# Performance work log

Measured on AMD Instinct MI355X. Metric: run time of the kernel, lower is better.

The kernel has to match this reference:

```python
import jax, jax.numpy as jnp
import numpy as np
from jax import lax

LATENT, HIDDEN, OUT = 64, 128, 64
B, T = 4096, 100


def setup_inputs() -> dict:
    key = jax.random.key(0)
    ks = jax.random.split(key, 12)
    s = lambda fan_in: 1.0 / np.sqrt(fan_in)
    u = lambda k, shape, fan_in: jax.random.uniform(k, shape, jnp.float32, -s(fan_in), s(fan_in))
    return {
        "z0": jax.random.normal(ks[0], (B, LATENT), jnp.float32),
        "t": jnp.arange(T, dtype=jnp.float32) * 0.01,  # increasing time grid
        "fc1_w": u(ks[1], (HIDDEN, LATENT), LATENT), "fc1_b": u(ks[2], (HIDDEN,), LATENT),
        "fc2_w": u(ks[3], (HIDDEN, HIDDEN), HIDDEN), "fc2_b": u(ks[4], (HIDDEN,), HIDDEN),
        "fc3_w": u(ks[5], (LATENT, HIDDEN), HIDDEN), "fc3_b": u(ks[6], (LATENT,), HIDDEN),
        "l2h_w": u(ks[7], (HIDDEN, LATENT), LATENT), "l2h_b": u(ks[8], (HIDDEN,), LATENT),
        "h2o_w": u(ks[9], (OUT, HIDDEN), HIDDEN), "h2o_b": u(ks[10], (OUT,), HIDDEN),
    }


def reference(z0, t, fc1_w, fc1_b, fc2_w, fc2_b, fc3_w, fc3_b, l2h_w, l2h_b, h2o_w, h2o_b):
    elu = jax.nn.elu

    def f(z):  # ODE_Func: fc1-elu-fc2-elu-fc3
        h = elu(z @ fc1_w.T + fc1_b)
        h = elu(h @ fc2_w.T + fc2_b)
        return h @ fc3_w.T + fc3_b

    dts = t[1:] - t[:-1]  # [T-1]

    def step(z, dt):  # fixed-step RK4
        k1 = f(z)
        k2 = f(z + 0.5 * dt * k1)
        k3 = f(z + 0.5 * dt * k2)
        k4 = f(z + dt * k3)
        zn = z + (dt / 6.0) * (k1 + 2.0 * k2 + 2.0 * k3 + k4)
        return zn, zn

    _, zs = lax.scan(step, z0, dts)          # [T-1, B, latent]
    pred_z = jnp.concatenate([z0[None], zs], axis=0)  # whole sequence [T, B, latent]
    # decode: h2o(relu(l2h(pred_z)))
    h = jax.nn.relu(pred_z @ l2h_w.T + l2h_b)
    return h @ h2o_w.T + h2o_b               # [T, B, out]
```

## Files before the change

### kernel.cpp

```cpp
#include <hip/hip_runtime.h>

typedef _Float16 f16;
typedef _Float16 f16x4 __attribute__((ext_vector_type(4)));
typedef _Float16 f16x8 __attribute__((ext_vector_type(8)));
typedef __fp16   h16x2 __attribute__((ext_vector_type(2)));
typedef float    f32x4 __attribute__((ext_vector_type(4)));

struct h16x2x2 { h16x2 lo, hi; };

#define MFMA16(a,b,c) __builtin_amdgcn_mfma_f32_16x16x32_f16((a),(b),(c),0,0,0)

#define LATENT 64
#define HIDDEN 128
#define ROWB  272
#define ROWF  (ROWB / 2)

__device__ __forceinline__ void bar_lds() {
  asm volatile("s_waitcnt lgkmcnt(0)\n\ts_barrier" ::: "memory");
}

__device__ __forceinline__ f16x8 load_afrag(const float* __restrict__ W, int K,
                                            int tile, int kf, int lane) {
  const int row = tile * 16 + (lane & 15);
  const int k0  = kf * 32 + (lane >> 4) * 8;
  const float* p = W + row * K + k0;
  f16x8 r;
#pragma unroll
  for (int j = 0; j < 8; ++j) r[j] = (f16)p[j];
  return r;
}

__device__ __forceinline__ f16x8 bfrag(const f16* buf, int k0, int lane) {
  const int b  = lane & 15;
  const int kk = k0 + (lane >> 4) * 8;
  return *(const f16x8*)((const char*)buf + b * ROWB + kk * 2);
}

__device__ __forceinline__ void dwrite(f16* buf, int dbase, f32x4 v, int lane) {
  const int b = lane & 15;
  h16x2x2 p;
  p.lo = __builtin_amdgcn_cvt_pkrtz(v[0], v[1]);
  p.hi = __builtin_amdgcn_cvt_pkrtz(v[2], v[3]);
  const f16x4 h = __builtin_bit_cast(f16x4, p);
  *(f16x4*)((char*)buf + b * ROWB + dbase * 2) = h;
}

__device__ __forceinline__ f32x4 elu4(f32x4 d) {
#pragma unroll
  for (int i = 0; i < 4; ++i) {
    const float e = __expf(d[i]) - 1.f;
    d[i] = d[i] > 0.f ? d[i] : e;
  }
  return d;
}

__global__ __launch_bounds__(256, 2)
void node_rk4_kernel(const float* __restrict__ z0,   const float* __restrict__ tg,
                     const float* __restrict__ fc1w, const float* __restrict__ fc1b,
                     const float* __restrict__ fc2w, const float* __restrict__ fc2b,
                     const float* __restrict__ fc3w, const float* __restrict__ fc3b,
                     const float* __restrict__ l2hw, const float* __restrict__ l2hb,
                     const float* __restrict__ h2ow, const float* __restrict__ h2ob,
                     float* __restrict__ out, int Btot, int T) {
  __shared__ __align__(16) f16 xbuf[16 * ROWF];
  __shared__ __align__(16) f16 h1buf[16 * ROWF];
  __shared__ __align__(16) f16 h2buf[16 * ROWF];
  __shared__ __align__(16) f16 dch1[16 * ROWF];

  const int tid  = threadIdx.x;
  const int lane = tid & 63;
  const int wv   = tid >> 6;
  const int grp  = lane >> 4;
  const int bcol = lane & 15;
  const int row0 = blockIdx.x * 16;
  const f32x4 Z0 = {0.f, 0.f, 0.f, 0.f};

  f16x8 a1[2][2], aL[2][2], a2[2][4], a3[4], aO[4];
  f32x4 b1[2], b2[2], bL[2], b3, bO;
#pragma unroll
  for (int ot = 0; ot < 2; ++ot) {
#pragma unroll
    for (int kf = 0; kf < 2; ++kf) {
      a1[ot][kf] = load_afrag(fc1w, 64, 2 * wv + ot, kf, lane);
      aL[ot][kf] = load_afrag(l2hw, 64, 2 * wv + ot, kf, lane);
    }
#pragma unroll
    for (int kf = 0; kf < 4; ++kf) a2[ot][kf] = load_afrag(fc2w, 128, 2 * wv + ot, kf, lane);
    const int d = (2 * wv + ot) * 16 + grp * 4;
    b1[ot] = *(const f32x4*)(fc1b + d);
    b2[ot] = *(const f32x4*)(fc2b + d);
    bL[ot] = *(const f32x4*)(l2hb + d);
  }
#pragma unroll
  for (int kf = 0; kf < 4; ++kf) {
    a3[kf] = load_afrag(fc3w, 128, wv, kf, lane);
    aO[kf] = load_afrag(h2ow, 128, wv, kf, lane);
  }
  const int dz = wv * 16 + grp * 4;
  b3 = *(const f32x4*)(fc3b + dz);
  bO = *(const f32x4*)(h2ob + dz);

  f32x4 z = *(const f32x4*)(z0 + (size_t)(row0 + bcol) * LATENT + dz);

  auto l1 = [&](f16x8 v0, f16x8 v1) {
#pragma unroll
    for (int ot = 0; ot < 2; ++ot) {
      f32x4 d = MFMA16(a1[ot][0], v0, b1[ot]);
      d = MFMA16(a1[ot][1], v1, d);
      d = elu4(d);
      dwrite(h1buf, (2 * wv + ot) * 16 + grp * 4, d, lane);
    }
  };
  auto l2 = [&]() {
    f16x8 h[4];
#pragma unroll
    for (int kf = 0; kf < 4; ++kf) h[kf] = bfrag(h1buf, kf * 32, lane);
#pragma unroll
    for (int ot = 0; ot < 2; ++ot) {
      f32x4 c0 = MFMA16(a2[ot][0], h[0], b2[ot]);
      c0 = MFMA16(a2[ot][1], h[1], c0);
      f32x4 c1 = MFMA16(a2[ot][2], h[2], Z0);
      c1 = MFMA16(a2[ot][3], h[3], c1);
      f32x4 d = elu4(c0 + c1);
      dwrite(h2buf, (2 * wv + ot) * 16 + grp * 4, d, lane);
    }
  };
  auto l3 = [&]() -> f32x4 {
    f16x8 g[4];
#pragma unroll
    for (int kf = 0; kf < 4; ++kf) g[kf] = bfrag(h2buf, kf * 32, lane);
    f32x4 c0 = MFMA16(a3[0], g[0], b3);
    c0 = MFMA16(a3[1], g[1], c0);
    f32x4 c1 = MFMA16(a3[2], g[2], Z0);
    c1 = MFMA16(a3[3], g[3], c1);
    return c0 + c1;
  };
  auto dec2_store = [&](int s) {
    f16x8 hd[4];
#pragma unroll
    for (int kf = 0; kf < 4; ++kf) hd[kf] = bfrag(dch1, kf * 32, lane);
    f32x4 c0 = MFMA16(aO[0], hd[0], bO);
    c0 = MFMA16(aO[1], hd[1], c0);
    f32x4 c1 = MFMA16(aO[2], hd[2], Z0);
    c1 = MFMA16(aO[3], hd[3], c1);
    f32x4 o = c0 + c1;
    *(f32x4*)(out + ((size_t)s * Btot + row0 + bcol) * LATENT + dz) = o;
  };

  dwrite(xbuf, dz, z, lane);
  bar_lds();

  float t_cur = tg[0];
  float t_nxt = tg[1];
  for (int s = 0;; ++s) {
    const bool last = (s == T - 1);

    {
      const f16x8 x0 = bfrag(xbuf, 0, lane);
      const f16x8 x1 = bfrag(xbuf, 32, lane);
#pragma unroll
      for (int ot = 0; ot < 2; ++ot) {
        f32x4 d = MFMA16(aL[ot][0], x0, bL[ot]);
        d = MFMA16(aL[ot][1], x1, d);
#pragma unroll
        for (int i = 0; i < 4; ++i) d[i] = fmaxf(d[i], 0.f);
        dwrite(dch1, (2 * wv + ot) * 16 + grp * 4, d, lane);
      }
      if (!last) l1(x0, x1);
    }
    bar_lds();

    if (last) { dec2_store(s); break; }

    l2();
    bar_lds();

    const float t_fut = tg[s + 2 < T ? s + 2 : T - 1];
    const float dt = t_nxt - t_cur;
    f32x4 k, acc, xs;

    dec2_store(s);
    k = l3();
    acc = k;
#pragma unroll
    for (int i = 0; i < 4; ++i) xs[i] = z[i] + 0.5f * dt * k[i];
    dwrite(xbuf, dz, xs, lane);
    bar_lds();

    { const f16x8 x0 = bfrag(xbuf, 0, lane), x1 = bfrag(xbuf, 32, lane);
      l1(x0, x1); }
    bar_lds();
    l2();
    bar_lds();
    k = l3();
#pragma unroll
    for (int i = 0; i < 4; ++i) { acc[i] += 2.f * k[i]; xs[i] = z[i] + 0.5f * dt * k[i]; }
    dwrite(xbuf, dz, xs, lane);
    bar_lds();

    { const f16x8 x0 = bfrag(xbuf, 0, lane), x1 = bfrag(xbuf, 32, lane);
      l1(x0, x1); }
    bar_lds();
    l2();
    bar_lds();
    k = l3();
#pragma unroll
    for (int i = 0; i < 4; ++i) { acc[i] += 2.f * k[i]; xs[i] = z[i] + dt * k[i]; }
    dwrite(xbuf, dz, xs, lane);
    bar_lds();

    { const f16x8 x0 = bfrag(xbuf, 0, lane), x1 = bfrag(xbuf, 32, lane);
      l1(x0, x1); }
    bar_lds();
    l2();
    bar_lds();
    k = l3();
#pragma unroll
    for (int i = 0; i < 4; ++i) z[i] += (dt / 6.f) * (acc[i] + k[i]);
    dwrite(xbuf, dz, z, lane);
    bar_lds();

    t_cur = t_nxt;
    t_nxt = t_fut;
  }
}

extern "C" void kernel_launch(void* const* d_in, const int* in_sizes, int n_in,
                              void* d_out, int out_size, void* d_ws, size_t ws_size,
                              hipStream_t stream) {
  const float* z0   = (const float*)d_in[0];
  const float* tg   = (const float*)d_in[1];
  const float* fc1w = (const float*)d_in[2];
  const float* fc1b = (const float*)d_in[3];
  const float* fc2w = (const float*)d_in[4];
  const float* fc2b = (const float*)d_in[5];
  const float* fc3w = (const float*)d_in[6];
  const float* fc3b = (const float*)d_in[7];
  const float* l2hw = (const float*)d_in[8];
  const float* l2hb = (const float*)d_in[9];
  const float* h2ow = (const float*)d_in[10];
  const float* h2ob = (const float*)d_in[11];
  float* out = (float*)d_out;

  const int Btot = in_sizes[0] / LATENT;
  const int T    = in_sizes[1];

  dim3 grid(Btot / 16), block(256);
  node_rk4_kernel<<<grid, block, 0, stream>>>(z0, tg, fc1w, fc1b, fc2w, fc2b,
                                              fc3w, fc3b, l2hw, l2hb, h2ow, h2ob,
                                              out, Btot, T);
}
```

Measured before the change: 298.2 us.

## Fold fc3 into fc1 and decoder l2h to track pre-activations instead of z

Precomputes the fused matrices fc1·fc3 and l2h·fc3, plus the bias vectors fc1·b3 and l2h·b3, in the prologue. The RK4 stages then update the fc1 and l2h pre-activations directly from the hidden layer-2 activations, so the separate fc3 and per-stage fc1 GEMMs disappear. The RK4 weighted sum is accumulated in f16 hidden space and applied once per step. This removes one GEMM and barrier pair per stage, but accumulates drift in pre-activation space with f16 rounding of the fused weights and stage sums. Launch bounds drop to one block per SIMD slot, to make room for the larger register footprint.

```diff
diff --git a/kernel.cpp b/kernel.cpp
--- a/kernel.cpp
+++ b/kernel.cpp
@@ -17,6 +17,9 @@
 
 __device__ __forceinline__ void bar_lds() {
   asm volatile("s_waitcnt lgkmcnt(0)\n\ts_barrier" ::: "memory");
+}
+__device__ __forceinline__ void fence_lds() {
+  asm volatile("s_waitcnt lgkmcnt(0)" ::: "memory");
 }
 
 __device__ __forceinline__ f16x8 load_afrag(const float* __restrict__ W, int K,
@@ -54,7 +57,7 @@
   return d;
 }
 
-__global__ __launch_bounds__(256, 2)
+__global__ __launch_bounds__(256, 1)
 void node_rk4_kernel(const float* __restrict__ z0,   const float* __restrict__ tg,
                      const float* __restrict__ fc1w, const float* __restrict__ fc1b,
                      const float* __restrict__ fc2w, const float* __restrict__ fc2b,
@@ -62,9 +65,9 @@
                      const float* __restrict__ l2hw, const float* __restrict__ l2hb,
                      const float* __restrict__ h2ow, const float* __restrict__ h2ob,
                      float* __restrict__ out, int Btot, int T) {
-  __shared__ __align__(16) f16 xbuf[16 * ROWF];
   __shared__ __align__(16) f16 h1buf[16 * ROWF];
-  __shared__ __align__(16) f16 h2buf[16 * ROWF];
+  __shared__ __align__(16) f16 h2a[16 * ROWF];
+  __shared__ __align__(16) f16 h2b[16 * ROWF];
   __shared__ __align__(16) f16 dch1[16 * ROWF];
 
   const int tid  = threadIdx.x;
@@ -75,43 +78,104 @@
   const int row0 = blockIdx.x * 16;
   const f32x4 Z0 = {0.f, 0.f, 0.f, 0.f};
 
-  f16x8 a1[2][2], aL[2][2], a2[2][4], a3[4], aO[4];
-  f32x4 b1[2], b2[2], bL[2], b3, bO;
+  f16x8 a2[2][4], aO[4];
+  f32x4 b2[2], bO;
 #pragma unroll
   for (int ot = 0; ot < 2; ++ot) {
 #pragma unroll
+    for (int kf = 0; kf < 4; ++kf) a2[ot][kf] = load_afrag(fc2w, 128, 2 * wv + ot, kf, lane);
+    b2[ot] = *(const f32x4*)(fc2b + (2 * wv + ot) * 16 + grp * 4);
+  }
+  const int dz = wv * 16 + grp * 4;
+#pragma unroll
+  for (int kf = 0; kf < 4; ++kf) aO[kf] = load_afrag(h2ow, 128, wv, kf, lane);
+  bO = *(const f32x4*)(h2ob + dz);
+
+  {
+    f32x4 zv = *(const f32x4*)(z0 + (size_t)(row0 + bcol) * LATENT + dz);
+    dwrite(h2a, dz, zv, lane);
+  }
+  bar_lds();
+
+  f16x8 a1t[2][2], aLt[2][2];
+  f32x4 b1t[2], bLt[2];
+#pragma unroll
+  for (int ot = 0; ot < 2; ++ot) {
+#pragma unroll
     for (int kf = 0; kf < 2; ++kf) {
-      a1[ot][kf] = load_afrag(fc1w, 64, 2 * wv + ot, kf, lane);
-      aL[ot][kf] = load_afrag(l2hw, 64, 2 * wv + ot, kf, lane);
-    }
-#pragma unroll
-    for (int kf = 0; kf < 4; ++kf) a2[ot][kf] = load_afrag(fc2w, 128, 2 * wv + ot, kf, lane);
-    const int d = (2 * wv + ot) * 16 + grp * 4;
-    b1[ot] = *(const f32x4*)(fc1b + d);
-    b2[ot] = *(const f32x4*)(fc2b + d);
-    bL[ot] = *(const f32x4*)(l2hb + d);
-  }
-#pragma unroll
-  for (int kf = 0; kf < 4; ++kf) {
-    a3[kf] = load_afrag(fc3w, 128, wv, kf, lane);
-    aO[kf] = load_afrag(h2ow, 128, wv, kf, lane);
-  }
-  const int dz = wv * 16 + grp * 4;
-  b3 = *(const f32x4*)(fc3b + dz);
-  bO = *(const f32x4*)(h2ob + dz);
-
-  f32x4 z = *(const f32x4*)(z0 + (size_t)(row0 + bcol) * LATENT + dz);
-
-  auto l1 = [&](f16x8 v0, f16x8 v1) {
-#pragma unroll
-    for (int ot = 0; ot < 2; ++ot) {
-      f32x4 d = MFMA16(a1[ot][0], v0, b1[ot]);
-      d = MFMA16(a1[ot][1], v1, d);
-      d = elu4(d);
-      dwrite(h1buf, (2 * wv + ot) * 16 + grp * 4, d, lane);
-    }
-  };
-  auto l2 = [&]() {
+      a1t[ot][kf] = load_afrag(fc1w, 64, 2 * wv + ot, kf, lane);
+      aLt[ot][kf] = load_afrag(l2hw, 64, 2 * wv + ot, kf, lane);
+    }
+    b1t[ot] = *(const f32x4*)(fc1b + (2 * wv + ot) * 16 + grp * 4);
+    bLt[ot] = *(const f32x4*)(l2hb + (2 * wv + ot) * 16 + grp * 4);
+  }
+
+  f32x4 pre1[2], preL[2];
+  {
+    const f16x8 zf0 = bfrag(h2a, 0, lane);
+    const f16x8 zf1 = bfrag(h2a, 32, lane);
+#pragma unroll
+    for (int ot = 0; ot < 2; ++ot) {
+      pre1[ot] = MFMA16(a1t[ot][1], zf1, MFMA16(a1t[ot][0], zf0, b1t[ot]));
+      preL[ot] = MFMA16(aLt[ot][1], zf1, MFMA16(aLt[ot][0], zf0, bLt[ot]));
+    }
+  }
+  bar_lds();
+
+  f32x4 v13[2], vL3[2];
+#pragma unroll
+  for (int ot = 0; ot < 2; ++ot) {
+#pragma unroll
+    for (int r = 0; r < 4; ++r) {
+      const int dimg = (2 * wv + ot) * 16 + grp * 4 + r;
+      float s13 = 0.f, sL3 = 0.f;
+      for (int l = 0; l < LATENT; l += 4) {
+        const f32x4 bv = *(const f32x4*)(fc3b + l);
+        const f32x4 w1 = *(const f32x4*)(fc1w + dimg * LATENT + l);
+        const f32x4 wL = *(const f32x4*)(l2hw + dimg * LATENT + l);
+#pragma unroll
+        for (int q = 0; q < 4; ++q) { s13 += w1[q] * bv[q]; sL3 += wL[q] * bv[q]; }
+      }
+      v13[ot][r] = s13;
+      vL3[ot][r] = sL3;
+    }
+  }
+
+  f16* scr = wv == 0 ? h1buf : wv == 1 ? h2a : wv == 2 ? h2b : dch1;
+  f16x8 w13[2][4], wL3[2][4];
+#pragma unroll
+  for (int m = 0; m < 2; ++m) {
+#pragma unroll
+    for (int ot = 0; ot < 2; ++ot) {
+      for (int tj = 0; tj < 8; ++tj) {
+        f16x8 bf0, bf1;
+#pragma unroll
+        for (int jj = 0; jj < 8; ++jj) {
+          const int l0 = 8 * grp + jj;
+          bf0[jj] = (f16)fc3w[l0 * HIDDEN + 16 * tj + bcol];
+          bf1[jj] = (f16)fc3w[(32 + l0) * HIDDEN + 16 * tj + bcol];
+        }
+        f32x4 d;
+        if (m == 0) d = MFMA16(a1t[ot][1], bf1, MFMA16(a1t[ot][0], bf0, Z0));
+        else        d = MFMA16(aLt[ot][1], bf1, MFMA16(aLt[ot][0], bf0, Z0));
+#pragma unroll
+        for (int r = 0; r < 4; ++r)
+          scr[(4 * grp + r) * ROWF + 16 * tj + bcol] = (f16)d[r];
+      }
+      fence_lds();
+      if (m == 0) {
+#pragma unroll
+        for (int kf = 0; kf < 4; ++kf) w13[ot][kf] = bfrag(scr, kf * 32, lane);
+      } else {
+#pragma unroll
+        for (int kf = 0; kf < 4; ++kf) wL3[ot][kf] = bfrag(scr, kf * 32, lane);
+      }
+      fence_lds();
+    }
+  }
+  bar_lds();
+
+  auto l2 = [&](f16* dst) {
     f16x8 h[4];
 #pragma unroll
     for (int kf = 0; kf < 4; ++kf) h[kf] = bfrag(h1buf, kf * 32, lane);
@@ -122,104 +186,108 @@
       f32x4 c1 = MFMA16(a2[ot][2], h[2], Z0);
       c1 = MFMA16(a2[ot][3], h[3], c1);
       f32x4 d = elu4(c0 + c1);
-      dwrite(h2buf, (2 * wv + ot) * 16 + grp * 4, d, lane);
+      dwrite(dst, (2 * wv + ot) * 16 + grp * 4, d, lane);
     }
   };
-  auto l3 = [&]() -> f32x4 {
-    f16x8 g[4];
-#pragma unroll
-    for (int kf = 0; kf < 4; ++kf) g[kf] = bfrag(h2buf, kf * 32, lane);
-    f32x4 c0 = MFMA16(a3[0], g[0], b3);
-    c0 = MFMA16(a3[1], g[1], c0);
-    f32x4 c1 = MFMA16(a3[2], g[2], Z0);
-    c1 = MFMA16(a3[3], g[3], c1);
-    return c0 + c1;
+
+  f16x8 hs0, hs1, hs2, hs3;
+
+  auto stageW = [&](const f16* src, float sc, int mode ) {
+    f16x8 h0 = bfrag(src, 0, lane),  h1f = bfrag(src, 32, lane);
+    f16x8 h2f = bfrag(src, 64, lane), h3f = bfrag(src, 96, lane);
+    if (mode == 0) { hs0 = h0; hs1 = h1f; hs2 = h2f; hs3 = h3f; }
+    else { hs0 += h0 + h0; hs1 += h1f + h1f; hs2 += h2f + h2f; hs3 += h3f + h3f; }
+#pragma unroll
+    for (int ot = 0; ot < 2; ++ot) {
+      f32x4 c0 = MFMA16(w13[ot][0], h0, v13[ot]);
+      c0 = MFMA16(w13[ot][1], h1f, c0);
+      f32x4 c1 = MFMA16(w13[ot][2], h2f, Z0);
+      c1 = MFMA16(w13[ot][3], h3f, c1);
+      f32x4 pk;
+#pragma unroll
+      for (int i = 0; i < 4; ++i) pk[i] = pre1[ot][i] + sc * (c0[i] + c1[i]);
+      pk = elu4(pk);
+      dwrite(h1buf, (2 * wv + ot) * 16 + grp * 4, pk, lane);
+    }
   };
-  auto dec2_store = [&](int s) {
-    f16x8 hd[4];
-#pragma unroll
-    for (int kf = 0; kf < 4; ++kf) hd[kf] = bfrag(dch1, kf * 32, lane);
-    f32x4 c0 = MFMA16(aO[0], hd[0], bO);
-    c0 = MFMA16(aO[1], hd[1], c0);
-    f32x4 c1 = MFMA16(aO[2], hd[2], Z0);
-    c1 = MFMA16(aO[3], hd[3], c1);
-    f32x4 o = c0 + c1;
-    *(f32x4*)(out + ((size_t)s * Btot + row0 + bcol) * LATENT + dz) = o;
-  };
-
-  dwrite(xbuf, dz, z, lane);
-  bar_lds();
 
   float t_cur = tg[0];
   float t_nxt = tg[1];
+  float dtp = 0.f, dt6p = 0.f;
   for (int s = 0;; ++s) {
     const bool last = (s == T - 1);
 
+    if (s > 0) {
+      hs0 += bfrag(h2b, 0, lane);
+      hs1 += bfrag(h2b, 32, lane);
+      hs2 += bfrag(h2b, 64, lane);
+      hs3 += bfrag(h2b, 96, lane);
+#pragma unroll
+      for (int ot = 0; ot < 2; ++ot) {
+        f32x4 c0 = MFMA16(w13[ot][0], hs0, Z0);
+        c0 = MFMA16(w13[ot][1], hs1, c0);
+        f32x4 c1 = MFMA16(w13[ot][2], hs2, Z0);
+        c1 = MFMA16(w13[ot][3], hs3, c1);
+#pragma unroll
+        for (int i = 0; i < 4; ++i) pre1[ot][i] += dt6p * (c0[i] + c1[i]) + dtp * v13[ot][i];
+        f32x4 d0 = MFMA16(wL3[ot][0], hs0, Z0);
+        d0 = MFMA16(wL3[ot][1], hs1, d0);
+        f32x4 d1 = MFMA16(wL3[ot][2], hs2, Z0);
+        d1 = MFMA16(wL3[ot][3], hs3, d1);
+#pragma unroll
+        for (int i = 0; i < 4; ++i) preL[ot][i] += dt6p * (d0[i] + d1[i]) + dtp * vL3[ot][i];
+      }
+    }
+#pragma unroll
+    for (int ot = 0; ot < 2; ++ot) {
+      f32x4 d;
+#pragma unroll
+      for (int i = 0; i < 4; ++i) d[i] = fmaxf(preL[ot][i], 0.f);
+      dwrite(dch1, (2 * wv + ot) * 16 + grp * 4, d, lane);
+    }
+    if (!last) {
+#pragma unroll
+      for (int ot = 0; ot < 2; ++ot) {
+        f32x4 d = elu4(pre1[ot]);
+        dwrite(h1buf, (2 * wv + ot) * 16 + grp * 4, d, lane);
+      }
+    }
+    bar_lds();
+
     {
-      const f16x8 x0 = bfrag(xbuf, 0, lane);
-      const f16x8 x1 = bfrag(xbuf, 32, lane);
-#pragma unroll
-      for (int ot = 0; ot < 2; ++ot) {
-        f32x4 d = MFMA16(aL[ot][0], x0, bL[ot]);
-        d = MFMA16(aL[ot][1], x1, d);
-#pragma unroll
-        for (int i = 0; i < 4; ++i) d[i] = fmaxf(d[i], 0.f);
-        dwrite(dch1, (2 * wv + ot) * 16 + grp * 4, d, lane);
-      }
-      if (!last) l1(x0, x1);
-    }
-    bar_lds();
-
-    if (last) { dec2_store(s); break; }
-
-    l2();
+      f16x8 hd[4];
+#pragma unroll
+      for (int kf = 0; kf < 4; ++kf) hd[kf] = bfrag(dch1, kf * 32, lane);
+      f32x4 c0 = MFMA16(aO[0], hd[0], bO);
+      c0 = MFMA16(aO[1], hd[1], c0);
+      f32x4 c1 = MFMA16(aO[2], hd[2], Z0);
+      c1 = MFMA16(aO[3], hd[3], c1);
+      f32x4 o = c0 + c1;
+      *(f32x4*)(out + ((size_t)s * Btot + row0 + bcol) * LATENT + dz) = o;
+      if (last) break;
+      l2(h2a);
+    }
     bar_lds();
 
     const float t_fut = tg[s + 2 < T ? s + 2 : T - 1];
     const float dt = t_nxt - t_cur;
-    f32x4 k, acc, xs;
-
-    dec2_store(s);
-    k = l3();
-    acc = k;
-#pragma unroll
-    for (int i = 0; i < 4; ++i) xs[i] = z[i] + 0.5f * dt * k[i];
-    dwrite(xbuf, dz, xs, lane);
-    bar_lds();
-
-    { const f16x8 x0 = bfrag(xbuf, 0, lane), x1 = bfrag(xbuf, 32, lane);
-      l1(x0, x1); }
-    bar_lds();
-    l2();
-    bar_lds();
-    k = l3();
-#pragma unroll
-    for (int i = 0; i < 4; ++i) { acc[i] += 2.f * k[i]; xs[i] = z[i] + 0.5f * dt * k[i]; }
-    dwrite(xbuf, dz, xs, lane);
-    bar_lds();
-
-    { const f16x8 x0 = bfrag(xbuf, 0, lane), x1 = bfrag(xbuf, 32, lane);
-      l1(x0, x1); }
-    bar_lds();
-    l2();
-    bar_lds();
-    k = l3();
-#pragma unroll
-    for (int i = 0; i < 4; ++i) { acc[i] += 2.f * k[i]; xs[i] = z[i] + dt * k[i]; }
-    dwrite(xbuf, dz, xs, lane);
-    bar_lds();
-
-    { const f16x8 x0 = bfrag(xbuf, 0, lane), x1 = bfrag(xbuf, 32, lane);
-      l1(x0, x1); }
-    bar_lds();
-    l2();
-    bar_lds();
-    k = l3();
-#pragma unroll
-    for (int i = 0; i < 4; ++i) z[i] += (dt / 6.f) * (acc[i] + k[i]);
-    dwrite(xbuf, dz, z, lane);
-    bar_lds();
-
+    const float hdt = 0.5f * dt;
+
+    stageW(h2a, hdt, 0);
+    bar_lds();
+    l2(h2b);
+    bar_lds();
+    stageW(h2b, hdt, 1);
+    bar_lds();
+    l2(h2a);
+    bar_lds();
+    stageW(h2a, dt, 1);
+    bar_lds();
+    l2(h2b);
+    bar_lds();
+
+    dtp = dt;
+    dt6p = dt * (1.f / 6.f);
     t_cur = t_nxt;
     t_nxt = t_fut;
   }
```

New measurement: 405.4 us. +35.9%, slower.
